# Kernel tuning notes

Hardware: AMD Instinct MI355X
Metric: run time of the kernel (lower is better)

The kernel has to match this reference:

```python
import jax, jax.numpy as jnp
import numpy as np

B, N, D, H, C, TOPK = 1, 1024, 1024, 16, 64, 2
HD = D // H   # head_dim = 64
G = N // C    # num blocks = 16


def setup_inputs() -> dict:
    key = jax.random.key(0)
    ks = jax.random.split(key, 6)
    s = 0.02  # init_std
    x = jax.random.normal(ks[0], (B, N, D), jnp.float32)
    Wq = jax.random.normal(ks[1], (D, D), jnp.float32) * s
    Wk = jax.random.normal(ks[2], (D, D), jnp.float32) * s
    Wv = jax.random.normal(ks[3], (D, D), jnp.float32) * s
    Wg = jax.random.normal(ks[4], (2 * H, D), jnp.float32) * s
    Wo = jax.random.normal(ks[5], (D, D), jnp.float32) * s
    return {"x": x, "Wq": Wq, "Wk": Wk, "Wv": Wv, "Wg": Wg, "Wo": Wo}


def reference(x, Wq, Wk, Wv, Wg, Wo):
    b, n, d = x.shape
    h, c, hd, g = H, C, HD, G
    scale = hd ** -0.5
    # projections (torch Linear: x @ W.T)
    q = (x @ Wq.T).reshape(b, n, h, hd)
    k = (x @ Wk.T).reshape(b, n, h, hd)
    v = (x @ Wv.T).reshape(b, n, h, hd)
    gate = jax.nn.softmax((x @ Wg.T).reshape(b, n, h, 2), axis=-1)
    # chunked views: (b, g, c, h, hd)
    kc = k.reshape(b, g, c, h, hd)
    vc = v.reshape(b, g, c, h, hd)
    # compressed block keys: mean over chunk dim -> (b, g, h, hd)
    k_compress = kc.mean(axis=2)
    # block selection scores (b, h, n, g)
    score = jnp.einsum('bnhd,bghd->bhng', q, k_compress)
    pos = jnp.arange(n)[:, None]
    blk = jnp.arange(g)[None, :]
    mask = pos >= c * blk  # (n, g), exactly as source's _get_mask (masked_fill where True)
    score = jnp.where(mask[None, None], -jnp.inf, score)
    idx = jax.lax.top_k(score, TOPK)[1]  # (b, h, n, top_k), int indices
    # gather selected blocks per (batch, head, query)
    k_bhgcd = kc.transpose(0, 3, 1, 2, 4)  # (b, h, g, c, hd)
    v_bhgcd = vc.transpose(0, 3, 1, 2, 4)
    gather = jax.vmap(jax.vmap(lambda kv, i: kv[i]))  # over b, h
    k_sel = gather(k_bhgcd, idx).reshape(b, h, n, TOPK * c, hd)
    v_sel = gather(v_bhgcd, idx).reshape(b, h, n, TOPK * c, hd)
    # inter: per-query attention over gathered KV (non-causal), flash-attn scale 1/sqrt(hd)
    logits = jnp.einsum('bnhd,bhnld->bhnl', q, k_sel) * scale
    p = jax.nn.softmax(logits, axis=-1)
    o_inter = jnp.einsum('bhnl,bhnld->bnhd', p, v_sel)
    # intra: causal attention within each chunk
    qc = q.reshape(b, g, c, h, hd)
    intra = jnp.einsum('bgihd,bgjhd->bghij', qc, kc) * scale
    cm = jnp.tril(jnp.ones((c, c), dtype=bool))
    intra = jnp.where(cm, intra, -jnp.inf)
    pi = jax.nn.softmax(intra, axis=-1)
    o_intra = jnp.einsum('bghij,bgjhd->bgihd', pi, vc).reshape(b, n, h, hd)
    # gated blend + output projection
    o = gate[..., 0:1] * o_inter + gate[..., 1:2] * o_intra  # (b, n, h, hd)
    return o.reshape(b, n, h * hd) @ Wo.T
```

## Files before the change

kernel.cpp:

```cpp
#include <hip/hip_runtime.h>
#include <hip/hip_bf16.h>
#include <math.h>


typedef __attribute__((ext_vector_type(8))) short short8;
typedef __attribute__((ext_vector_type(4))) float f32x4;

#define NTOK 1024
#define DMODEL 1024
#define NHEAD 16
#define HDIM 64
#define CHUNK 64
#define NBLK 16

__device__ __forceinline__ float qmax16(float v)
{
    #pragma unroll
    for (int off = 1; off < 16; off <<= 1) v = fmaxf(v, __shfl_xor(v, off));
    return v;
}

__device__ __forceinline__ float qsum16(float v)
{
    #pragma unroll
    for (int off = 1; off < 16; off <<= 1) v += __shfl_xor(v, off);
    return v;
}


#define GLOAD_LDS16(gp, lp)                                              \
    __builtin_amdgcn_global_load_lds(                                    \
        (const __attribute__((address_space(1))) void*)(gp),             \
        (__attribute__((address_space(3))) void*)(lp), 16, 0, 0)

__device__ __forceinline__ void stage64(const __hip_bfloat16* __restrict__ g0,
                                        __hip_bfloat16* t, int wave, int lane)
{
    const int sub = lane >> 3;
    const int cch = (lane & 7) ^ sub;
    #pragma unroll
    for (int j = 0; j < 2; j++) {
        const int rr = (2 * wave + j) * 8 + sub;
        GLOAD_LDS16(g0 + (size_t)rr * DMODEL + cch * 8, t + (2 * wave + j) * 512);
    }
}

__device__ __forceinline__ void stage128(const __hip_bfloat16* __restrict__ g0,
                                         __hip_bfloat16* t, int wave, int lane)
{
    const int sub = lane >> 3;
    const int cch = (lane & 7) ^ sub;
    #pragma unroll
    for (int j = 0; j < 4; j++) {
        const int grp = wave * 4 + j;
        GLOAD_LDS16(g0 + (size_t)(grp * 8 + sub) * DMODEL + cch * 8, t + grp * 512);
    }
}

__device__ __forceinline__ void stage64w8(const __hip_bfloat16* __restrict__ g0,
                                          __hip_bfloat16* t, int wave, int lane)
{
    const int sub = lane >> 3;
    const int cch = (lane & 7) ^ sub;
    GLOAD_LDS16(g0 + (size_t)(wave * 8 + sub) * DMODEL + cch * 8, t + wave * 512);
}

__device__ __forceinline__ short8 ldsfrag(const __hip_bfloat16* t, int row, int chunk)
{
    return *(const short8*)((const char*)t + row * 128 + (((chunk) ^ (row & 7)) << 4));
}

__global__ __launch_bounds__(256) void prep_kernel(
    const float* __restrict__ x,  const float* __restrict__ Wq,
    const float* __restrict__ Wk, const float* __restrict__ Wv,
    const float* __restrict__ Wo, const float* __restrict__ Wg,
    __hip_bfloat16* __restrict__ xh,  __hip_bfloat16* __restrict__ xl,
    __hip_bfloat16* __restrict__ Wqh,
    __hip_bfloat16* __restrict__ Wkh, __hip_bfloat16* __restrict__ Wvh,
    __hip_bfloat16* __restrict__ Woh, __hip_bfloat16* __restrict__ Wol,
    float* __restrict__ xm, float2* __restrict__ gate)
{
    __shared__ float gs[32];
    const int bid = blockIdx.x;
    if (bid < 5120) {
        const int which = bid >> 10;
        const int b = bid & 1023;
        const int i = (b * 256 + threadIdx.x) * 4;
        const float* in; __hip_bfloat16 *hi, *lo = nullptr;
        if (which == 0)      { in = x;  hi = xh;  lo = xl; }
        else if (which == 1) { in = Wq; hi = Wqh; }
        else if (which == 2) { in = Wk; hi = Wkh; }
        else if (which == 3) { in = Wv; hi = Wvh; }
        else                 { in = Wo; hi = Woh; lo = Wol; }
        float4 v = *(const float4*)(in + i);
        float vv[4] = {v.x, v.y, v.z, v.w};
        __hip_bfloat16 h[4], l[4];
        #pragma unroll
        for (int j = 0; j < 4; j++) {
            h[j] = __float2bfloat16(vv[j]);
            l[j] = __float2bfloat16(vv[j] - __bfloat162float(h[j]));
        }
        *(uint2*)(hi + i) = *(uint2*)h;
        if (lo) *(uint2*)(lo + i) = *(uint2*)l;
    } else if (bid < 5184) {
        const int b = bid - 5120;
        const int g = b >> 2;
        const int f = (b & 3) * 256 + threadIdx.x;
        float s = 0.f;
        #pragma unroll 8
        for (int c = 0; c < CHUNK; c++) s += x[(size_t)(g * CHUNK + c) * DMODEL + f];
        xm[g * DMODEL + f] = s * (1.0f / CHUNK);
    } else {
        const int n = bid - 5184;
        const int wave = threadIdx.x >> 6, lane = threadIdx.x & 63;
        #pragma unroll
        for (int jj = 0; jj < 8; jj++) {
            int j = wave * 8 + jj;
            float s = 0.f;
            #pragma unroll
            for (int t = 0; t < 16; t++) {
                int d = lane + (t << 6);
                s += x[n * DMODEL + d] * Wg[j * DMODEL + d];
            }
            #pragma unroll
            for (int off = 32; off; off >>= 1) s += __shfl_xor(s, off);
            if (lane == 0) gs[j] = s;
        }
        __syncthreads();
        if (threadIdx.x < NHEAD) {
            int h = threadIdx.x;
            float a = gs[2 * h], b = gs[2 * h + 1];
            float m = fmaxf(a, b);
            float ea = expf(a - m), eb = expf(b - m);
            float inv = 1.f / (ea + eb);
            gate[n * NHEAD + h] = make_float2(ea * inv, eb * inv);
        }
    }
}

__global__ __launch_bounds__(256) void kc_gemm_kernel(
    const float* __restrict__ xm, const float* __restrict__ Wk,
    float* __restrict__ kc)
{
    const int f = blockIdx.x;
    const int g = threadIdx.x >> 4;
    const int sub = threadIdx.x & 15;
    const float* wrow = Wk + (size_t)f * DMODEL;
    float s = 0.f;
    #pragma unroll 16
    for (int i = 0; i < 64; i++) {
        int e = i * 16 + sub;
        s += xm[g * DMODEL + e] * wrow[e];
    }
    #pragma unroll
    for (int off = 8; off; off >>= 1) s += __shfl_xor(s, off);
    if (sub == 0) kc[g * DMODEL + f] = s;
}

__global__ __launch_bounds__(256) void u_kernel(
    const float* __restrict__ kc, const float* __restrict__ Wq,
    __hip_bfloat16* __restrict__ Uh, __hip_bfloat16* __restrict__ Ul)
{
    __shared__ float kcs[64];
    const int h = blockIdx.x >> 4, g = blockIdx.x & 15;
    if (threadIdx.x < 64) kcs[threadIdx.x] = kc[g * DMODEL + h * HDIM + threadIdx.x];
    __syncthreads();
    const int col = (h << 4) | g;
    for (int f = threadIdx.x; f < DMODEL; f += 256) {
        float s = 0.f;
        #pragma unroll 16
        for (int d = 0; d < 64; d++)
            s += kcs[d] * Wq[(size_t)(h * HDIM + d) * DMODEL + f];
        __hip_bfloat16 hv = __float2bfloat16(s);
        Uh[(size_t)col * DMODEL + f] = hv;
        Ul[(size_t)col * DMODEL + f] = __float2bfloat16(s - __bfloat162float(hv));
    }
}

__global__ __launch_bounds__(256) void qkv_score_kernel(
    const __hip_bfloat16* __restrict__ xh, const __hip_bfloat16* __restrict__ xl,
    const __hip_bfloat16* __restrict__ Wqh, const __hip_bfloat16* __restrict__ Wkh,
    const __hip_bfloat16* __restrict__ Wvh,
    const __hip_bfloat16* __restrict__ Uh, const __hip_bfloat16* __restrict__ Ul,
    __hip_bfloat16* __restrict__ Qb, __hip_bfloat16* __restrict__ Kb,
    __hip_bfloat16* __restrict__ Vt, float* __restrict__ S)
{
    __shared__ alignas(16) char smem[65536];

    const int b = blockIdx.x;
    const int tid  = threadIdx.x;
    const int wave = tid >> 6;
    const int lane = tid & 63;
    const int fr = lane & 15;
    const int quad = lane >> 4;

    if (b < 192) {
        __hip_bfloat16* A0 = (__hip_bfloat16*)smem;
        __hip_bfloat16* B0 = (__hip_bfloat16*)(smem + 16384);
        __hip_bfloat16* A1 = (__hip_bfloat16*)(smem + 32768);
        __hip_bfloat16* B1 = (__hip_bfloat16*)(smem + 49152);

        const int widx = b >> 6;
        const int t = b & 63;
        const int m0 = (t >> 3) * 128;
        const int n0 = (t & 7) * 128;
        const __hip_bfloat16* __restrict__ Bw =
            (widx == 0) ? Wqh : (widx == 1) ? Wkh : Wvh;

        const int wm = (wave >> 1) * 64;
        const int wn = (wave & 1) * 64;

        f32x4 acc[4][4] = {};

        stage128(xh + (size_t)m0 * DMODEL, A0, wave, lane);
        stage128(Bw + (size_t)n0 * DMODEL, B0, wave, lane);
        asm volatile("s_waitcnt vmcnt(0)" ::: "memory");
        __builtin_amdgcn_sched_barrier(0);
        __builtin_amdgcn_s_barrier();

        for (int kt = 0; kt < 16; kt++) {
            const int cur = kt & 1;
            __hip_bfloat16* Ac = cur ? A1 : A0;
            __hip_bfloat16* Bc = cur ? B1 : B0;
            if (kt < 15) {
                __hip_bfloat16* An = cur ? A0 : A1;
                __hip_bfloat16* Bn = cur ? B0 : B1;
                stage128(xh + (size_t)m0 * DMODEL + (kt + 1) * 64, An, wave, lane);
                stage128(Bw + (size_t)n0 * DMODEL + (kt + 1) * 64, Bn, wave, lane);
                asm volatile("s_waitcnt vmcnt(8)" ::: "memory");
            } else {
                asm volatile("s_waitcnt vmcnt(0)" ::: "memory");
            }
            __builtin_amdgcn_sched_barrier(0);
            __builtin_amdgcn_s_barrier();
            __builtin_amdgcn_sched_barrier(0);

            #pragma unroll
            for (int hk = 0; hk < 2; hk++) {
                const int ch = hk * 4 + quad;
                short8 am[4], bn[4];
                #pragma unroll
                for (int i = 0; i < 4; i++) am[i] = ldsfrag(Ac, wm + i * 16 + fr, ch);
                #pragma unroll
                for (int j = 0; j < 4; j++) bn[j] = ldsfrag(Bc, wn + j * 16 + fr, ch);
                #pragma unroll
                for (int i = 0; i < 4; i++)
                #pragma unroll
                for (int j = 0; j < 4; j++)
                    acc[i][j] = __builtin_amdgcn_mfma_f32_16x16x32_bf16(am[i], bn[j], acc[i][j], 0, 0, 0);
            }
            __builtin_amdgcn_sched_barrier(0);
            __builtin_amdgcn_s_barrier();
            __builtin_amdgcn_sched_barrier(0);
        }

        if (widx == 0 || widx == 1) {
            __hip_bfloat16* __restrict__ Out = (widx == 0) ? Qb : Kb;
            #pragma unroll
            for (int i = 0; i < 4; i++)
            #pragma unroll
            for (int j = 0; j < 4; j++)
            #pragma unroll
            for (int r = 0; r < 4; r++) {
                int row = m0 + wm + i * 16 + quad * 4 + r;
                int col = n0 + wn + j * 16 + fr;
                Out[(size_t)row * DMODEL + col] = __float2bfloat16(acc[i][j][r]);
            }
        } else {
            __hip_bfloat16 (*T)[136] = (__hip_bfloat16(*)[136])smem;
            for (int p = 0; p < 2; p++) {
                __syncthreads();
                if ((wn >> 6) == p) {
                    #pragma unroll
                    for (int i = 0; i < 4; i++)
                    #pragma unroll
                    for (int j = 0; j < 4; j++)
                    #pragma unroll
                    for (int r = 0; r < 4; r++) {
                        int nloc = wm + i * 16 + quad * 4 + r;
                        int floc = (wn - p * 64) + j * 16 + fr;
                        T[floc][nloc] = __float2bfloat16(acc[i][j][r]);
                    }
                }
                __syncthreads();
                const int row = tid >> 2;
                const int cb  = (tid & 3) * 32;
                const size_t o = (size_t)(n0 + p * 64 + row) * NTOK + m0 + cb;
                #pragma unroll
                for (int u = 0; u < 4; u++)
                    *(uint4*)(Vt + o + u * 8) = *(uint4*)(&T[row][cb + u * 8]);
            }
        }
    } else {
        __hip_bfloat16* AshP = (__hip_bfloat16*)smem;
        __hip_bfloat16* AslP = (__hip_bfloat16*)(smem + 8192);
        __hip_bfloat16* BshP = (__hip_bfloat16*)(smem + 16384);
        __hip_bfloat16* BslP = (__hip_bfloat16*)(smem + 24576);

        const int wm = (wave >> 1) * 32;
        const int wn = (wave & 1) * 32;

        const int bb = b - 192;
        const int m0 = (bb >> 2) * 64;
        const int n0 = (bb & 3) * 64;

        f32x4 acc[2][2] = {};

        for (int k0 = 0; k0 < DMODEL; k0 += 64) {
            stage64(xh + (size_t)m0 * DMODEL + k0, AshP, wave, lane);
            stage64(xl + (size_t)m0 * DMODEL + k0, AslP, wave, lane);
            stage64(Uh + (size_t)n0 * DMODEL + k0, BshP, wave, lane);
            stage64(Ul + (size_t)n0 * DMODEL + k0, BslP, wave, lane);
            __syncthreads();

            #pragma unroll
            for (int hk = 0; hk < 2; hk++) {
                const int ch = hk * 4 + quad;
                short8 a0h = ldsfrag(AshP, wm + fr, ch);
                short8 a1h = ldsfrag(AshP, wm + 16 + fr, ch);
                short8 a0l = ldsfrag(AslP, wm + fr, ch);
                short8 a1l = ldsfrag(AslP, wm + 16 + fr, ch);
                short8 b0h = ldsfrag(BshP, wn + fr, ch);
                short8 b1h = ldsfrag(BshP, wn + 16 + fr, ch);
                short8 b0l = ldsfrag(BslP, wn + fr, ch);
                short8 b1l = ldsfrag(BslP, wn + 16 + fr, ch);
                acc[0][0] = __builtin_amdgcn_mfma_f32_16x16x32_bf16(a0l, b0h, acc[0][0], 0, 0, 0);
                acc[0][1] = __builtin_amdgcn_mfma_f32_16x16x32_bf16(a0l, b1h, acc[0][1], 0, 0, 0);
                acc[1][0] = __builtin_amdgcn_mfma_f32_16x16x32_bf16(a1l, b0h, acc[1][0], 0, 0, 0);
                acc[1][1] = __builtin_amdgcn_mfma_f32_16x16x32_bf16(a1l, b1h, acc[1][1], 0, 0, 0);
                acc[0][0] = __builtin_amdgcn_mfma_f32_16x16x32_bf16(a0h, b0l, acc[0][0], 0, 0, 0);
                acc[0][1] = __builtin_amdgcn_mfma_f32_16x16x32_bf16(a0h, b1l, acc[0][1], 0, 0, 0);
                acc[1][0] = __builtin_amdgcn_mfma_f32_16x16x32_bf16(a1h, b0l, acc[1][0], 0, 0, 0);
                acc[1][1] = __builtin_amdgcn_mfma_f32_16x16x32_bf16(a1h, b1l, acc[1][1], 0, 0, 0);
                acc[0][0] = __builtin_amdgcn_mfma_f32_16x16x32_bf16(a0h, b0h, acc[0][0], 0, 0, 0);
                acc[0][1] = __builtin_amdgcn_mfma_f32_16x16x32_bf16(a0h, b1h, acc[0][1], 0, 0, 0);
                acc[1][0] = __builtin_amdgcn_mfma_f32_16x16x32_bf16(a1h, b0h, acc[1][0], 0, 0, 0);
                acc[1][1] = __builtin_amdgcn_mfma_f32_16x16x32_bf16(a1h, b1h, acc[1][1], 0, 0, 0);
            }
            __syncthreads();
        }

        #pragma unroll
        for (int tm = 0; tm < 2; tm++)
        #pragma unroll
        for (int tn = 0; tn < 2; tn++)
        #pragma unroll
        for (int r = 0; r < 4; r++) {
            int row = m0 + wm + tm * 16 + quad * 4 + r;
            int col = n0 + wn + tn * 16 + fr;
            S[(size_t)row * 256 + col] = acc[tm][tn][r];
        }
    }
}

__global__ __launch_bounds__(256, 4) void attn_mfma_kernel(
    const __hip_bfloat16* __restrict__ Qb, const __hip_bfloat16* __restrict__ Kb,
    const __hip_bfloat16* __restrict__ Vt, const float* __restrict__ S,
    const float2* __restrict__ gate, __hip_bfloat16* __restrict__ oh)
{
    __shared__ float OS[4][16][64];
    __shared__ float OIs[16][64];
    __shared__ float mS[4][16], lS[4][16], liS[16];
    __shared__ int i1s[16], i2s[16];
    __shared__ float2 sgate[16];
    __shared__ unsigned unionMask;
    __shared__ __hip_bfloat16 Ps[4][16][72];

    const int bid = blockIdx.x;
    const int qt = bid & 3;
    const int h  = (bid >> 2) & 15;
    const int g  = bid >> 6;
    const int tid = threadIdx.x;
    const int s = tid >> 6;
    const int lane = tid & 63;
    const int fr = lane & 15, quad = lane >> 4;

    if (tid < 16) {
        const int n = g * 64 + qt * 16 + tid;
        const float* Sn = S + (size_t)n * 256 + h * 16;
        float sc[NBLK];
        #pragma unroll
        for (int gg = 0; gg < NBLK; gg++)
            sc[gg] = (n >= (gg << 6)) ? -INFINITY : Sn[gg];
        int i1 = -1, i2 = -1;
        float b1 = -INFINITY;
        #pragma unroll
        for (int gg = 0; gg < NBLK; gg++) if (i1 < 0 || sc[gg] > b1) { b1 = sc[gg]; i1 = gg; }
        float b2 = -INFINITY;
        #pragma unroll
        for (int gg = 0; gg < NBLK; gg++) { if (gg == i1) continue; if (i2 < 0 || sc[gg] > b2) { b2 = sc[gg]; i2 = gg; } }
        i1s[tid] = i1; i2s[tid] = i2;
        sgate[tid] = gate[(size_t)n * NHEAD + h];
        unsigned m = (1u << i1) | (1u << i2);
        #pragma unroll
        for (int off = 1; off < 16; off <<= 1) m |= (unsigned)__shfl_xor((int)m, off);
        if (tid == 0) unionMask = m;
    }
    __syncthreads();

    const unsigned um = unionMask;

    const size_t qrow = (size_t)(g * 64 + qt * 16 + fr) * DMODEL + h * HDIM + quad * 8;
    const short8 qa0 = *(const short8*)(Qb + qrow);
    const short8 qa1 = *(const short8*)(Qb + qrow + 32);

    int qi1[4], qi2[4];
    #pragma unroll
    for (int r = 0; r < 4; r++) {
        int q = quad * 4 + r;
        qi1[r] = i1s[q]; qi2[r] = i2s[q];
    }

    f32x4 Oint[4] = {};
    float mrun[4] = {-INFINITY, -INFINITY, -INFINITY, -INFINITY};
    float lrun[4] = {0.f, 0.f, 0.f, 0.f};

    const __hip_bfloat16* __restrict__ Kh = Kb + h * HDIM + quad * 8;
    const __hip_bfloat16* __restrict__ Vh = Vt + (size_t)(h * HDIM) * NTOK + quad * 8;

    int j = 0;
    for (int kb = 0; kb < NBLK; kb++) {
        if (!((um >> kb) & 1u)) continue;
        if ((j++ & 3) != s) continue;

        f32x4 sacc[4] = {};
        #pragma unroll
        for (int t = 0; t < 4; t++) {
            const size_t krow = (size_t)(kb * 64 + t * 16 + fr) * DMODEL;
            short8 kb0 = *(const short8*)(Kh + krow);
            short8 kb1 = *(const short8*)(Kh + krow + 32);
            sacc[t] = __builtin_amdgcn_mfma_f32_16x16x32_bf16(qa0, kb0, sacc[t], 0, 0, 0);
            sacc[t] = __builtin_amdgcn_mfma_f32_16x16x32_bf16(qa1, kb1, sacc[t], 0, 0, 0);
        }

        #pragma unroll
        for (int r = 0; r < 4; r++) {
            const bool sel = (kb == qi1[r]) | (kb == qi2[r]);
            float v0 = sacc[0][r] * 0.125f, v1 = sacc[1][r] * 0.125f;
            float v2 = sacc[2][r] * 0.125f, v3 = sacc[3][r] * 0.125f;
            float mx = qmax16(fmaxf(fmaxf(v0, v1), fmaxf(v2, v3)));
            float mnew = sel ? fmaxf(mrun[r], mx) : mrun[r];
            float f = sel ? __expf(mrun[r] - mnew) : 1.0f;
            float e0 = sel ? __expf(v0 - mnew) : 0.f;
            float e1 = sel ? __expf(v1 - mnew) : 0.f;
            float e2 = sel ? __expf(v2 - mnew) : 0.f;
            float e3 = sel ? __expf(v3 - mnew) : 0.f;
            float es = qsum16(e0 + e1 + e2 + e3);
            lrun[r] = lrun[r] * f + es;
            mrun[r] = mnew;
            #pragma unroll
            for (int dn = 0; dn < 4; dn++) Oint[dn][r] *= f;
            const int prow = quad * 4 + r;
            Ps[s][prow][ 0 + fr] = __float2bfloat16(e0);
            Ps[s][prow][16 + fr] = __float2bfloat16(e1);
            Ps[s][prow][32 + fr] = __float2bfloat16(e2);
            Ps[s][prow][48 + fr] = __float2bfloat16(e3);
        }

        short8 pa0 = *(const short8*)(&Ps[s][fr][quad * 8]);
        short8 pa1 = *(const short8*)(&Ps[s][fr][32 + quad * 8]);
        #pragma unroll
        for (int dn = 0; dn < 4; dn++) {
            const size_t vrow = (size_t)(dn * 16 + fr) * NTOK + kb * 64;
            short8 v0 = *(const short8*)(Vh + vrow);
            short8 v1 = *(const short8*)(Vh + vrow + 32);
            Oint[dn] = __builtin_amdgcn_mfma_f32_16x16x32_bf16(pa0, v0, Oint[dn], 0, 0, 0);
            Oint[dn] = __builtin_amdgcn_mfma_f32_16x16x32_bf16(pa1, v1, Oint[dn], 0, 0, 0);
        }
    }

    if ((j & 3) == s) {
        f32x4 sacc[4] = {};
        #pragma unroll
        for (int t = 0; t < 4; t++) {
            const size_t krow = (size_t)(g * 64 + t * 16 + fr) * DMODEL;
            short8 kb0 = *(const short8*)(Kh + krow);
            short8 kb1 = *(const short8*)(Kh + krow + 32);
            sacc[t] = __builtin_amdgcn_mfma_f32_16x16x32_bf16(qa0, kb0, sacc[t], 0, 0, 0);
            sacc[t] = __builtin_amdgcn_mfma_f32_16x16x32_bf16(qa1, kb1, sacc[t], 0, 0, 0);
        }
        f32x4 Ointr[4] = {};
        #pragma unroll
        for (int r = 0; r < 4; r++) {
            const int qloc = qt * 16 + quad * 4 + r;
            float vv[4];
            #pragma unroll
            for (int t = 0; t < 4; t++) {
                const int col = t * 16 + fr;
                float v = sacc[t][r] * 0.125f;
                vv[t] = (col <= qloc) ? v : -INFINITY;
            }
            float mx = qmax16(fmaxf(fmaxf(vv[0], vv[1]), fmaxf(vv[2], vv[3])));
            float e0 = __expf(vv[0] - mx), e1 = __expf(vv[1] - mx);
            float e2 = __expf(vv[2] - mx), e3 = __expf(vv[3] - mx);
            float lsum = qsum16(e0 + e1 + e2 + e3);
            const int prow = quad * 4 + r;
            if (fr == 0) liS[prow] = lsum;
            Ps[s][prow][ 0 + fr] = __float2bfloat16(e0);
            Ps[s][prow][16 + fr] = __float2bfloat16(e1);
            Ps[s][prow][32 + fr] = __float2bfloat16(e2);
            Ps[s][prow][48 + fr] = __float2bfloat16(e3);
        }
        short8 pa0 = *(const short8*)(&Ps[s][fr][quad * 8]);
        short8 pa1 = *(const short8*)(&Ps[s][fr][32 + quad * 8]);
        f32x4 Ointr2[4] = {};
        #pragma unroll
        for (int dn = 0; dn < 4; dn++) {
            const size_t vrow = (size_t)(dn * 16 + fr) * NTOK + g * 64;
            short8 v0 = *(const short8*)(Vh + vrow);
            short8 v1 = *(const short8*)(Vh + vrow + 32);
            Ointr2[dn] = __builtin_amdgcn_mfma_f32_16x16x32_bf16(pa0, v0, Ointr[dn], 0, 0, 0);
            Ointr2[dn] = __builtin_amdgcn_mfma_f32_16x16x32_bf16(pa1, v1, Ointr2[dn], 0, 0, 0);
        }
        #pragma unroll
        for (int r = 0; r < 4; r++)
        #pragma unroll
        for (int dn = 0; dn < 4; dn++)
            OIs[quad * 4 + r][dn * 16 + fr] = Ointr2[dn][r];
    }

    #pragma unroll
    for (int r = 0; r < 4; r++) {
        if (fr == 0) { mS[s][quad * 4 + r] = mrun[r]; lS[s][quad * 4 + r] = lrun[r]; }
        #pragma unroll
        for (int dn = 0; dn < 4; dn++)
            OS[s][quad * 4 + r][dn * 16 + fr] = Oint[dn][r];
    }
    __syncthreads();

    {
        const int q = tid >> 4;
        const int db = (tid & 15) * 4;
        float M = fmaxf(fmaxf(mS[0][q], mS[1][q]), fmaxf(mS[2][q], mS[3][q]));
        float L = 0.f;
        float o0 = 0.f, o1 = 0.f, o2 = 0.f, o3 = 0.f;
        #pragma unroll
        for (int ss = 0; ss < 4; ss++) {
            float p = __expf(mS[ss][q] - M);
            L += lS[ss][q] * p;
            o0 += OS[ss][q][db + 0] * p;
            o1 += OS[ss][q][db + 1] * p;
            o2 += OS[ss][q][db + 2] * p;
            o3 += OS[ss][q][db + 3] * p;
        }
        const float2 gt = sgate[q];
        const float wi = gt.x / L;
        const float wl = gt.y / liS[q];
        unsigned short out4[4];
        out4[0] = __builtin_bit_cast(unsigned short, __float2bfloat16(wi * o0 + wl * OIs[q][db + 0]));
        out4[1] = __builtin_bit_cast(unsigned short, __float2bfloat16(wi * o1 + wl * OIs[q][db + 1]));
        out4[2] = __builtin_bit_cast(unsigned short, __float2bfloat16(wi * o2 + wl * OIs[q][db + 2]));
        out4[3] = __builtin_bit_cast(unsigned short, __float2bfloat16(wi * o3 + wl * OIs[q][db + 3]));
        const int n = g * 64 + qt * 16 + q;
        *(uint2*)(oh + (size_t)n * DMODEL + h * HDIM + db) = *(uint2*)out4;
    }
}

__global__ __launch_bounds__(512) void gemm_wo(
    const __hip_bfloat16* __restrict__ Ah,
    const __hip_bfloat16* __restrict__ Bh, const __hip_bfloat16* __restrict__ Bl,
    float* __restrict__ C)
{
    __shared__ alignas(16) char smem[49152];
    __hip_bfloat16* As0 = (__hip_bfloat16*)smem;
    __hip_bfloat16* Bh0 = (__hip_bfloat16*)(smem + 8192);
    __hip_bfloat16* Bl0 = (__hip_bfloat16*)(smem + 16384);
    __hip_bfloat16* As1 = (__hip_bfloat16*)(smem + 24576);
    __hip_bfloat16* Bh1 = (__hip_bfloat16*)(smem + 32768);
    __hip_bfloat16* Bl1 = (__hip_bfloat16*)(smem + 40960);

    const int n0 = blockIdx.x * 64;
    const int m0 = blockIdx.y * 64;

    const int tid  = threadIdx.x;
    const int wave = tid >> 6;
    const int lane = tid & 63;
    const int wm = (wave >> 1) * 16;
    const int wn = (wave & 1) * 32;
    const int fr = lane & 15;
    const int quad = lane >> 4;

    f32x4 acc[2] = {};

    stage64w8(Ah + (size_t)m0 * DMODEL, As0, wave, lane);
    stage64w8(Bh + (size_t)n0 * DMODEL, Bh0, wave, lane);
    stage64w8(Bl + (size_t)n0 * DMODEL, Bl0, wave, lane);
    asm volatile("s_waitcnt vmcnt(0)" ::: "memory");
    __builtin_amdgcn_sched_barrier(0);
    __builtin_amdgcn_s_barrier();

    for (int kt = 0; kt < 16; kt++) {
        const int cur = kt & 1;
        __hip_bfloat16* Ac  = cur ? As1 : As0;
        __hip_bfloat16* Bhc = cur ? Bh1 : Bh0;
        __hip_bfloat16* Blc = cur ? Bl1 : Bl0;
        if (kt < 15) {
            __hip_bfloat16* An  = cur ? As0 : As1;
            __hip_bfloat16* Bhn = cur ? Bh0 : Bh1;
            __hip_bfloat16* Bln = cur ? Bl0 : Bl1;
            stage64w8(Ah + (size_t)m0 * DMODEL + (kt + 1) * 64, An, wave, lane);
            stage64w8(Bh + (size_t)n0 * DMODEL + (kt + 1) * 64, Bhn, wave, lane);
            stage64w8(Bl + (size_t)n0 * DMODEL + (kt + 1) * 64, Bln, wave, lane);
            asm volatile("s_waitcnt vmcnt(3)" ::: "memory");
        } else {
            asm volatile("s_waitcnt vmcnt(0)" ::: "memory");
        }
        __builtin_amdgcn_sched_barrier(0);
        __builtin_amdgcn_s_barrier();
        __builtin_amdgcn_sched_barrier(0);

        #pragma unroll
        for (int hk = 0; hk < 2; hk++) {
            const int ch = hk * 4 + quad;
            short8 a0  = ldsfrag(Ac, wm + fr, ch);
            short8 b0h = ldsfrag(Bhc, wn + fr, ch);
            short8 b1h = ldsfrag(Bhc, wn + 16 + fr, ch);
            short8 b0l = ldsfrag(Blc, wn + fr, ch);
            short8 b1l = ldsfrag(Blc, wn + 16 + fr, ch);
            acc[0] = __builtin_amdgcn_mfma_f32_16x16x32_bf16(a0, b0l, acc[0], 0, 0, 0);
            acc[1] = __builtin_amdgcn_mfma_f32_16x16x32_bf16(a0, b1l, acc[1], 0, 0, 0);
            acc[0] = __builtin_amdgcn_mfma_f32_16x16x32_bf16(a0, b0h, acc[0], 0, 0, 0);
            acc[1] = __builtin_amdgcn_mfma_f32_16x16x32_bf16(a0, b1h, acc[1], 0, 0, 0);
        }
        __builtin_amdgcn_sched_barrier(0);
        __builtin_amdgcn_s_barrier();
        __builtin_amdgcn_sched_barrier(0);
    }

    #pragma unroll
    for (int tn = 0; tn < 2; tn++)
    #pragma unroll
    for (int r = 0; r < 4; r++) {
        int row = m0 + wm + quad * 4 + r;
        int col = n0 + wn + tn * 16 + fr;
        C[(size_t)row * DMODEL + col] = acc[tn][r];
    }
}

extern "C" void kernel_launch(void* const* d_in, const int* in_sizes, int n_in,
                              void* d_out, int out_size, void* d_ws, size_t ws_size,
                              hipStream_t stream)
{
    const float* x  = (const float*)d_in[0];
    const float* Wq = (const float*)d_in[1];
    const float* Wk = (const float*)d_in[2];
    const float* Wv = (const float*)d_in[3];
    const float* Wg = (const float*)d_in[4];
    const float* Wo = (const float*)d_in[5];

    const size_t M1 = (size_t)NTOK * DMODEL;

    float* S       = (float*)d_ws;
    float* xm      = S + (size_t)NTOK * 256;
    float* kc      = xm + NBLK * DMODEL;
    float2* gate   = (float2*)(kc + NBLK * DMODEL);
    __hip_bfloat16* xh  = (__hip_bfloat16*)(gate + NTOK * NHEAD);
    __hip_bfloat16* xl  = xh + M1;
    __hip_bfloat16* Wqh = xl + M1;
    __hip_bfloat16* Wkh = Wqh + M1;
    __hip_bfloat16* Wvh = Wkh + M1;
    __hip_bfloat16* Woh = Wvh + M1;
    __hip_bfloat16* Wol = Woh + M1;
    __hip_bfloat16* oh  = Wol + M1;
    __hip_bfloat16* Uh  = oh + M1;
    __hip_bfloat16* Ul  = Uh + 256 * DMODEL;
    __hip_bfloat16* Qb  = Ul + 256 * DMODEL;
    __hip_bfloat16* Kb  = Qb + M1;
    __hip_bfloat16* Vt  = Kb + M1;

    prep_kernel<<<6208, 256, 0, stream>>>(
        x, Wq, Wk, Wv, Wo, Wg, xh, xl, Wqh, Wkh, Wvh, Woh, Wol, xm, gate);

    kc_gemm_kernel<<<1024, 256, 0, stream>>>(xm, Wk, kc);
    u_kernel<<<256, 256, 0, stream>>>(kc, Wq, Uh, Ul);

    qkv_score_kernel<<<256, 256, 0, stream>>>(
        xh, xl, Wqh, Wkh, Wvh, Uh, Ul, Qb, Kb, Vt, S);

    attn_mfma_kernel<<<NBLK * NHEAD * 4, 256, 0, stream>>>(Qb, Kb, Vt, S, gate, oh);

    dim3 gwo(16, 16);
    gemm_wo<<<gwo, 512, 0, stream>>>(oh, Woh, Wol, (float*)d_out);
}
```

Measured before the change: 155.2 us.

## Move gate projection into MFMA score kernel and reuse Wq rows in u_kernel

The gate logits were computed in prep_kernel with one block per token doing scalar dot products. Now prep_kernel only splits Wg into bf16 hi/lo parts, and 16 extra blocks in qkv_score_kernel compute the gate with split-bf16 MFMA, applying the 2-way softmax in the epilogue. Separately, u_kernel now loads each Wq element once and applies it to 8 compressed-key groups, cutting repeated Wq reads in half the number of blocks. The price is more launch work for the score kernel and fewer, heavier u_kernel blocks.

Result: faster. 143.5 us (-7.5%).

```diff
diff --git a/kernel.cpp b/kernel.cpp
--- a/kernel.cpp
+++ b/kernel.cpp
@@ -78,9 +78,9 @@
     __hip_bfloat16* __restrict__ Wqh,
     __hip_bfloat16* __restrict__ Wkh, __hip_bfloat16* __restrict__ Wvh,
     __hip_bfloat16* __restrict__ Woh, __hip_bfloat16* __restrict__ Wol,
-    float* __restrict__ xm, float2* __restrict__ gate)
-{
-    __shared__ float gs[32];
+    __hip_bfloat16* __restrict__ Wgh, __hip_bfloat16* __restrict__ Wgl,
+    float* __restrict__ xm)
+{
     const int bid = blockIdx.x;
     if (bid < 5120) {
         const int which = bid >> 10;
@@ -111,30 +111,18 @@
         for (int c = 0; c < CHUNK; c++) s += x[(size_t)(g * CHUNK + c) * DMODEL + f];
         xm[g * DMODEL + f] = s * (1.0f / CHUNK);
     } else {
-        const int n = bid - 5184;
-        const int wave = threadIdx.x >> 6, lane = threadIdx.x & 63;
-        #pragma unroll
-        for (int jj = 0; jj < 8; jj++) {
-            int j = wave * 8 + jj;
-            float s = 0.f;
-            #pragma unroll
-            for (int t = 0; t < 16; t++) {
-                int d = lane + (t << 6);
-                s += x[n * DMODEL + d] * Wg[j * DMODEL + d];
-            }
-            #pragma unroll
-            for (int off = 32; off; off >>= 1) s += __shfl_xor(s, off);
-            if (lane == 0) gs[j] = s;
-        }
-        __syncthreads();
-        if (threadIdx.x < NHEAD) {
-            int h = threadIdx.x;
-            float a = gs[2 * h], b = gs[2 * h + 1];
-            float m = fmaxf(a, b);
-            float ea = expf(a - m), eb = expf(b - m);
-            float inv = 1.f / (ea + eb);
-            gate[n * NHEAD + h] = make_float2(ea * inv, eb * inv);
-        }
+        const int b = bid - 5184;
+        const int i = (b * 256 + threadIdx.x) * 4;
+        float4 v = *(const float4*)(Wg + i);
+        float vv[4] = {v.x, v.y, v.z, v.w};
+        __hip_bfloat16 h[4], l[4];
+        #pragma unroll
+        for (int j = 0; j < 4; j++) {
+            h[j] = __float2bfloat16(vv[j]);
+            l[j] = __float2bfloat16(vv[j] - __bfloat162float(h[j]));
+        }
+        *(uint2*)(Wgh + i) = *(uint2*)h;
+        *(uint2*)(Wgl + i) = *(uint2*)l;
     }
 }
 
@@ -161,16 +149,26 @@
     const float* __restrict__ kc, const float* __restrict__ Wq,
     __hip_bfloat16* __restrict__ Uh, __hip_bfloat16* __restrict__ Ul)
 {
-    __shared__ float kcs[64];
-    const int h = blockIdx.x >> 4, g = blockIdx.x & 15;
-    if (threadIdx.x < 64) kcs[threadIdx.x] = kc[g * DMODEL + h * HDIM + threadIdx.x];
+    __shared__ float kcs[16][64];
+    const int h = blockIdx.x >> 3, fs = blockIdx.x & 7;
+    for (int i = threadIdx.x; i < 1024; i += 256) {
+        int g = i >> 6, d = i & 63;
+        kcs[g][d] = kc[g * DMODEL + h * HDIM + d];
+    }
     __syncthreads();
-    const int col = (h << 4) | g;
-    for (int f = threadIdx.x; f < DMODEL; f += 256) {
-        float s = 0.f;
-        #pragma unroll 16
-        for (int d = 0; d < 64; d++)
-            s += kcs[d] * Wq[(size_t)(h * HDIM + d) * DMODEL + f];
+    const int f = fs * 128 + (threadIdx.x & 127);
+    const int gh = threadIdx.x >> 7;
+    float acc[8] = {};
+    for (int d = 0; d < 64; d++) {
+        float wv = Wq[(size_t)(h * HDIM + d) * DMODEL + f];
+        #pragma unroll
+        for (int gg = 0; gg < 8; gg++)
+            acc[gg] += kcs[gh * 8 + gg][d] * wv;
+    }
+    #pragma unroll
+    for (int gg = 0; gg < 8; gg++) {
+        const int col = (h << 4) | (gh * 8 + gg);
+        float s = acc[gg];
         __hip_bfloat16 hv = __float2bfloat16(s);
         Uh[(size_t)col * DMODEL + f] = hv;
         Ul[(size_t)col * DMODEL + f] = __float2bfloat16(s - __bfloat162float(hv));
@@ -182,8 +180,10 @@
     const __hip_bfloat16* __restrict__ Wqh, const __hip_bfloat16* __restrict__ Wkh,
     const __hip_bfloat16* __restrict__ Wvh,
     const __hip_bfloat16* __restrict__ Uh, const __hip_bfloat16* __restrict__ Ul,
+    const __hip_bfloat16* __restrict__ Wgh, const __hip_bfloat16* __restrict__ Wgl,
     __hip_bfloat16* __restrict__ Qb, __hip_bfloat16* __restrict__ Kb,
-    __hip_bfloat16* __restrict__ Vt, float* __restrict__ S)
+    __hip_bfloat16* __restrict__ Vt, float* __restrict__ S,
+    float2* __restrict__ gate)
 {
     __shared__ alignas(16) char smem[65536];
 
@@ -291,7 +291,7 @@
                     *(uint4*)(Vt + o + u * 8) = *(uint4*)(&T[row][cb + u * 8]);
             }
         }
-    } else {
+    } else if (b < 256) {
         __hip_bfloat16* AshP = (__hip_bfloat16*)smem;
         __hip_bfloat16* AslP = (__hip_bfloat16*)(smem + 8192);
         __hip_bfloat16* BshP = (__hip_bfloat16*)(smem + 16384);
@@ -350,6 +350,58 @@
             int col = n0 + wn + tn * 16 + fr;
             S[(size_t)row * 256 + col] = acc[tm][tn][r];
         }
+    } else {
+        __hip_bfloat16* AshP = (__hip_bfloat16*)smem;
+        __hip_bfloat16* AslP = (__hip_bfloat16*)(smem + 8192);
+        __hip_bfloat16* GhP  = (__hip_bfloat16*)(smem + 16384);
+        __hip_bfloat16* GlP  = (__hip_bfloat16*)(smem + 20480);
+
+        const int bb = b - 256;
+        const int m0 = bb * 64;
+
+        f32x4 acc[2] = {};
+
+        for (int k0 = 0; k0 < DMODEL; k0 += 64) {
+            stage64(xh + (size_t)m0 * DMODEL + k0, AshP, wave, lane);
+            stage64(xl + (size_t)m0 * DMODEL + k0, AslP, wave, lane);
+            stage64w8(Wgh + k0, GhP, wave, lane);
+            stage64w8(Wgl + k0, GlP, wave, lane);
+            __syncthreads();
+
+            #pragma unroll
+            for (int hk = 0; hk < 2; hk++) {
+                const int ch = hk * 4 + quad;
+                short8 ah  = ldsfrag(AshP, wave * 16 + fr, ch);
+                short8 al  = ldsfrag(AslP, wave * 16 + fr, ch);
+                short8 b0h = ldsfrag(GhP, fr, ch);
+                short8 b1h = ldsfrag(GhP, 16 + fr, ch);
+                short8 b0l = ldsfrag(GlP, fr, ch);
+                short8 b1l = ldsfrag(GlP, 16 + fr, ch);
+                acc[0] = __builtin_amdgcn_mfma_f32_16x16x32_bf16(al, b0h, acc[0], 0, 0, 0);
+                acc[1] = __builtin_amdgcn_mfma_f32_16x16x32_bf16(al, b1h, acc[1], 0, 0, 0);
+                acc[0] = __builtin_amdgcn_mfma_f32_16x16x32_bf16(ah, b0l, acc[0], 0, 0, 0);
+                acc[1] = __builtin_amdgcn_mfma_f32_16x16x32_bf16(ah, b1l, acc[1], 0, 0, 0);
+                acc[0] = __builtin_amdgcn_mfma_f32_16x16x32_bf16(ah, b0h, acc[0], 0, 0, 0);
+                acc[1] = __builtin_amdgcn_mfma_f32_16x16x32_bf16(ah, b1h, acc[1], 0, 0, 0);
+            }
+            __syncthreads();
+        }
+
+        #pragma unroll
+        for (int tn = 0; tn < 2; tn++)
+        #pragma unroll
+        for (int r = 0; r < 4; r++) {
+            float v = acc[tn][r];
+            float nb = __shfl_xor(v, 1);
+            if (!(fr & 1)) {
+                float m = fmaxf(v, nb);
+                float ea = expf(v - m), eb = expf(nb - m);
+                float inv = 1.f / (ea + eb);
+                const int hcol = tn * 8 + (fr >> 1);
+                const int row = m0 + wave * 16 + quad * 4 + r;
+                gate[(size_t)row * NHEAD + hcol] = make_float2(ea * inv, eb * inv);
+            }
+        }
     }
 }
 
@@ -667,15 +719,17 @@
     __hip_bfloat16* Qb  = Ul + 256 * DMODEL;
     __hip_bfloat16* Kb  = Qb + M1;
     __hip_bfloat16* Vt  = Kb + M1;
-
-    prep_kernel<<<6208, 256, 0, stream>>>(
-        x, Wq, Wk, Wv, Wo, Wg, xh, xl, Wqh, Wkh, Wvh, Woh, Wol, xm, gate);
+    __hip_bfloat16* Wgh = Vt + M1;
+    __hip_bfloat16* Wgl = Wgh + 32 * DMODEL;
+
+    prep_kernel<<<5216, 256, 0, stream>>>(
+        x, Wq, Wk, Wv, Wo, Wg, xh, xl, Wqh, Wkh, Wvh, Woh, Wol, Wgh, Wgl, xm);
 
     kc_gemm_kernel<<<1024, 256, 0, stream>>>(xm, Wk, kc);
-    u_kernel<<<256, 256, 0, stream>>>(kc, Wq, Uh, Ul);
-
-    qkv_score_kernel<<<256, 256, 0, stream>>>(
-        xh, xl, Wqh, Wkh, Wvh, Uh, Ul, Qb, Kb, Vt, S);
+    u_kernel<<<128, 256, 0, stream>>>(kc, Wq, Uh, Ul);
+
+    qkv_score_kernel<<<272, 256, 0, stream>>>(
+        xh, xl, Wqh, Wkh, Wvh, Uh, Ul, Wgh, Wgl, Qb, Kb, Vt, S, gate);
 
     attn_mfma_kernel<<<NBLK * NHEAD * 4, 256, 0, stream>>>(Qb, Kb, Vt, S, gate, oh);
 
```
